# Performance work log

Hardware: AMD Instinct MI355X
Metric: run time of the kernel (lower is better)

The kernel has to match this reference:

```python
import jax, jax.numpy as jnp
import numpy as np

N, E, F_IN, HID, EPS = 50000, 800000, 128, 256, 1e-5

def _glorot(key, shape):
    scale = 1.0 / np.sqrt(shape[0])
    return jax.random.uniform(key, shape, jnp.float32, -scale, scale)

def setup_inputs() -> dict:
    key = jax.random.key(0)
    ks = jax.random.split(key, 20)
    x = jax.random.normal(ks[0], (N, F_IN), jnp.float32)
    edge_index = jax.random.randint(ks[1], (2, E), 0, N, jnp.int64)
    inp = {"x": x, "edge_index": edge_index}
    dims = [F_IN, HID, HID]
    for i in range(3):
        d_in = dims[i]
        inp[f"Wn{i}"] = _glorot(ks[2 + 4 * i], (d_in, HID))      # lin_l weight (neighbors), with bias
        inp[f"bn{i}"] = jnp.zeros((HID,), jnp.float32)
        inp[f"Wr{i}"] = _glorot(ks[3 + 4 * i], (d_in, HID))      # lin_r weight (root), no bias
        inp[f"g{i}"] = jnp.ones((HID,), jnp.float32)              # BN gamma
        inp[f"b{i}"] = jnp.zeros((HID,), jnp.float32)             # BN beta
    return inp

def _sage_bn_elu(x, src, dst, Wn, bn, Wr, g, b):
    # mean aggregation of source features onto destination nodes
    agg = jax.ops.segment_sum(x[src], dst, num_segments=N)                      # [N, d_in]
    deg = jax.ops.segment_sum(jnp.ones((src.shape[0],), x.dtype), dst, num_segments=N)
    agg = agg / jnp.maximum(deg, 1.0)[:, None]
    h = agg @ Wn + bn + x @ Wr                                                  # SAGEConv(root_weight=True)
    mu = jnp.mean(h, axis=0)
    var = jnp.mean((h - mu) ** 2, axis=0)                                       # biased var (BN training)
    h = (h - mu) * jax.lax.rsqrt(var + EPS) * g + b
    return jnp.where(h > 0, h, jnp.expm1(h))                                    # ELU(alpha=1)

def reference(x, edge_index, Wn0, bn0, Wr0, g0, b0, Wn1, bn1, Wr1, g1, b1, Wn2, bn2, Wr2, g2, b2):
    src, dst = edge_index[0], edge_index[1]
    h = _sage_bn_elu(x, src, dst, Wn0, bn0, Wr0, g0, b0)
    h = _sage_bn_elu(h, src, dst, Wn1, bn1, Wr1, g1, b1)
    h = _sage_bn_elu(h, src, dst, Wn2, bn2, Wr2, g2, b2)
    return h
```

## Files before the change

kernel.cpp:

```cpp
#include <hip/hip_runtime.h>
#include <math.h>

#define N_NODES 50000
#define N_EDGES 800000
#define F_IN    128
#define HID     256
#define BN_EPS  1e-5f
#define SCAN_BLOCKS ((N_NODES + 255) / 256)
#define RB256       ((N_NODES + 255) / 256)
#define CAST_BLOCKS (N_NODES * F_IN / 4 / 256)
#define WT_BLOCKS   (16 + 32 + 32)

typedef unsigned int uint;
typedef __attribute__((ext_vector_type(8))) short bf16x8;
typedef __attribute__((ext_vector_type(4))) float f32x4;

__device__ __forceinline__ float bf2f(unsigned short u) {
    return __uint_as_float((uint)u << 16);
}
__device__ __forceinline__ unsigned short f2bf(float f) {
    uint u = __float_as_uint(f);
    return (unsigned short)((u + 0x7FFFu + ((u >> 16) & 1u)) >> 16);
}

__device__ __forceinline__ void gload16(const unsigned short* g, unsigned short* l) {
    __builtin_amdgcn_global_load_lds(
        (const __attribute__((address_space(1))) void*)g,
        (__attribute__((address_space(3))) void*)l, 16, 0, 0);
}

__device__ __forceinline__ void acc_u4(float* a, uint4 v) {
    a[0] += bf2f((unsigned short)(v.x & 0xFFFF)); a[1] += bf2f((unsigned short)(v.x >> 16));
    a[2] += bf2f((unsigned short)(v.y & 0xFFFF)); a[3] += bf2f((unsigned short)(v.y >> 16));
    a[4] += bf2f((unsigned short)(v.z & 0xFFFF)); a[5] += bf2f((unsigned short)(v.z >> 16));
    a[6] += bf2f((unsigned short)(v.w & 0xFFFF)); a[7] += bf2f((unsigned short)(v.w >> 16));
}
__device__ __forceinline__ void acc_u4m(float* a, uint4 v, float m) {
    a[0] += m * bf2f((unsigned short)(v.x & 0xFFFF)); a[1] += m * bf2f((unsigned short)(v.x >> 16));
    a[2] += m * bf2f((unsigned short)(v.y & 0xFFFF)); a[3] += m * bf2f((unsigned short)(v.y >> 16));
    a[4] += m * bf2f((unsigned short)(v.z & 0xFFFF)); a[5] += m * bf2f((unsigned short)(v.z >> 16));
    a[6] += m * bf2f((unsigned short)(v.w & 0xFFFF)); a[7] += m * bf2f((unsigned short)(v.w >> 16));
}

__global__ __launch_bounds__(256) void prep_kernel(
    const float* __restrict__ x, unsigned short* __restrict__ xb,
    const float* __restrict__ Wn0, const float* __restrict__ Wr0, unsigned short* __restrict__ WT0,
    const float* __restrict__ Wn1, const float* __restrict__ Wr1, unsigned short* __restrict__ WT1,
    const float* __restrict__ Wn2, const float* __restrict__ Wr2, unsigned short* __restrict__ WT2,
    int* __restrict__ deg) {
    int bb = blockIdx.x;
    if (bb < CAST_BLOCKS) {
        int i = bb * 256 + threadIdx.x;
        float4 v = *(const float4*)&x[(long)i * 4];
        unsigned short o[4] = {f2bf(v.x), f2bf(v.y), f2bf(v.z), f2bf(v.w)};
        *(uint2*)&xb[(long)i * 4] = *(const uint2*)o;
    } else if (bb < CAST_BLOCKS + SCAN_BLOCKS) {
        int i = (bb - CAST_BLOCKS) * 256 + threadIdx.x;
        if (i < N_NODES) deg[i] = 0;
    } else {
        int wb = bb - (CAST_BLOCKS + SCAN_BLOCKS);
        const float* Wn; const float* Wr; unsigned short* WT; int K1, KT, kb;
        if (wb < 16)      { Wn = Wn0; Wr = Wr0; WT = WT0; K1 = F_IN; KT = 2 * F_IN; kb = wb; }
        else if (wb < 48) { Wn = Wn1; Wr = Wr1; WT = WT1; K1 = HID;  KT = 2 * HID;  kb = wb - 16; }
        else              { Wn = Wn2; Wr = Wr2; WT = WT2; K1 = HID;  KT = 2 * HID;  kb = wb - 48; }
        int n  = threadIdx.x;
        int k0 = kb * 16;
        unsigned short o[16];
#pragma unroll
        for (int j = 0; j < 16; ++j) {
            int k = k0 + j;
            float v = (k < K1) ? Wn[k * HID + n] : Wr[(k - K1) * HID + n];
            o[j] = f2bf(v);
        }
        *(uint4*)&WT[(long)n * KT + k0]     = *(const uint4*)&o[0];
        *(uint4*)&WT[(long)n * KT + k0 + 8] = *(const uint4*)&o[8];
    }
}

__global__ void hist_kernel(const int* __restrict__ dst, int* __restrict__ deg,
                            int* __restrict__ rank) {
    int e = blockIdx.x * blockDim.x + threadIdx.x;
    if (e < N_EDGES) rank[e] = atomicAdd(&deg[dst[e]], 1);
}

__global__ __launch_bounds__(256) void scan1_kernel(const int* __restrict__ deg,
                                                    int* __restrict__ row_ptr,
                                                    int* __restrict__ partials) {
    __shared__ int sm[256];
    int i = blockIdx.x * 256 + threadIdx.x;
    int v = (i < N_NODES) ? deg[i] : 0;
    sm[threadIdx.x] = v;
    __syncthreads();
    for (int off = 1; off < 256; off <<= 1) {
        int t = (threadIdx.x >= off) ? sm[threadIdx.x - off] : 0;
        __syncthreads();
        sm[threadIdx.x] += t;
        __syncthreads();
    }
    if (i < N_NODES) row_ptr[i] = sm[threadIdx.x] - v;
    if (threadIdx.x == 255) partials[blockIdx.x] = sm[255];
}

__global__ __launch_bounds__(256) void scan3_kernel(int* __restrict__ row_ptr,
                                                    const int* __restrict__ partials) {
    __shared__ int red[4];
    int t = threadIdx.x;
    int v = (t < SCAN_BLOCKS && t < (int)blockIdx.x) ? partials[t] : 0;
#pragma unroll
    for (int off = 32; off; off >>= 1) v += __shfl_down(v, off);
    if ((t & 63) == 0) red[t >> 6] = v;
    __syncthreads();
    int base = red[0] + red[1] + red[2] + red[3];
    int i = blockIdx.x * 256 + t;
    if (i < N_NODES) row_ptr[i] += base;
    if (i == 0) row_ptr[N_NODES] = N_EDGES;
}

__global__ void fill_kernel(const int* __restrict__ src, const int* __restrict__ dst,
                            const int* __restrict__ rank, const int* __restrict__ row_ptr,
                            int* __restrict__ csr_src) {
    int e = blockIdx.x * blockDim.x + threadIdx.x;
    if (e >= N_EDGES) return;
    int pos = row_ptr[dst[e]] + rank[e];
    __builtin_nontemporal_store(src[e], &csr_src[pos]);
}

template<int D>
__global__ __launch_bounds__(256) void gather_mean_kernel(
    const unsigned short* __restrict__ x, const int* __restrict__ row_ptr,
    const int* __restrict__ csr_src, unsigned short* __restrict__ agg) {
    int node = blockIdx.x * 4 + (threadIdx.x >> 6);
    int lane = threadIdx.x & 63;
    if (node >= N_NODES) return;
    int beg = row_ptr[node], end = row_ptr[node + 1];
    float acc[8];
#pragma unroll
    for (int j = 0; j < 8; j++) acc[j] = 0.f;
    int e = beg;

    if constexpr (D == 256) {
        const int half = lane >> 5;
        const long lo  = (long)(lane & 31) * 8;
        for (; e + 16 <= end; e += 16) {
            int s0 = csr_src[e + half],      s1 = csr_src[e + 2 + half];
            int s2 = csr_src[e + 4 + half],  s3 = csr_src[e + 6 + half];
            int s4 = csr_src[e + 8 + half],  s5 = csr_src[e + 10 + half];
            int s6 = csr_src[e + 12 + half], s7 = csr_src[e + 14 + half];
            uint4 v0 = *(const uint4*)&x[(long)s0 * 256 + lo];
            uint4 v1 = *(const uint4*)&x[(long)s1 * 256 + lo];
            uint4 v2 = *(const uint4*)&x[(long)s2 * 256 + lo];
            uint4 v3 = *(const uint4*)&x[(long)s3 * 256 + lo];
            uint4 v4 = *(const uint4*)&x[(long)s4 * 256 + lo];
            uint4 v5 = *(const uint4*)&x[(long)s5 * 256 + lo];
            uint4 v6 = *(const uint4*)&x[(long)s6 * 256 + lo];
            uint4 v7 = *(const uint4*)&x[(long)s7 * 256 + lo];
            acc_u4(acc, v0); acc_u4(acc, v1); acc_u4(acc, v2); acc_u4(acc, v3);
            acc_u4(acc, v4); acc_u4(acc, v5); acc_u4(acc, v6); acc_u4(acc, v7);
        }
        for (; e + 8 <= end; e += 8) {
            int s0 = csr_src[e + half],     s1 = csr_src[e + 2 + half];
            int s2 = csr_src[e + 4 + half], s3 = csr_src[e + 6 + half];
            uint4 v0 = *(const uint4*)&x[(long)s0 * 256 + lo];
            uint4 v1 = *(const uint4*)&x[(long)s1 * 256 + lo];
            uint4 v2 = *(const uint4*)&x[(long)s2 * 256 + lo];
            uint4 v3 = *(const uint4*)&x[(long)s3 * 256 + lo];
            acc_u4(acc, v0); acc_u4(acc, v1); acc_u4(acc, v2); acc_u4(acc, v3);
        }
        for (; e + 2 <= end; e += 2) {
            int s0 = csr_src[e + half];
            uint4 v0 = *(const uint4*)&x[(long)s0 * 256 + lo];
            acc_u4(acc, v0);
        }
        if (e < end) {
            int s0 = csr_src[e];
            uint4 v0 = *(const uint4*)&x[(long)s0 * 256 + lo];
            acc_u4m(acc, v0, (half == 0) ? 1.f : 0.f);
        }
#pragma unroll
        for (int j = 0; j < 8; j++) acc[j] += __shfl_xor(acc[j], 32);
        float inv = 1.0f / fmaxf((float)(end - beg), 1.0f);
        if (half == 0) {
            unsigned short ov[8];
#pragma unroll
            for (int j = 0; j < 8; j++) ov[j] = f2bf(acc[j] * inv);
            *(uint4*)&agg[(long)node * 256 + lo] = *(const uint4*)ov;
        }
    } else {
        const int grp = lane >> 4;
        const long lo = (long)(lane & 15) * 8;
        for (; e + 16 <= end; e += 16) {
            int sA = csr_src[e + grp],     sB = csr_src[e + 4 + grp];
            int sC = csr_src[e + 8 + grp], sD = csr_src[e + 12 + grp];
            uint4 vA = *(const uint4*)&x[(long)sA * 128 + lo];
            uint4 vB = *(const uint4*)&x[(long)sB * 128 + lo];
            uint4 vC = *(const uint4*)&x[(long)sC * 128 + lo];
            uint4 vD = *(const uint4*)&x[(long)sD * 128 + lo];
            acc_u4(acc, vA); acc_u4(acc, vB); acc_u4(acc, vC); acc_u4(acc, vD);
        }
        for (; e + 8 <= end; e += 8) {
            int sA = csr_src[e + grp], sB = csr_src[e + 4 + grp];
            uint4 vA = *(const uint4*)&x[(long)sA * 128 + lo];
            uint4 vB = *(const uint4*)&x[(long)sB * 128 + lo];
            acc_u4(acc, vA); acc_u4(acc, vB);
        }
        for (; e + 4 <= end; e += 4) {
            int sA = csr_src[e + grp];
            uint4 vA = *(const uint4*)&x[(long)sA * 128 + lo];
            acc_u4(acc, vA);
        }
        for (; e < end; e++) {
            int s0 = csr_src[e];
            uint4 v0 = *(const uint4*)&x[(long)s0 * 128 + lo];
            acc_u4m(acc, v0, (grp == 0) ? 1.f : 0.f);
        }
#pragma unroll
        for (int j = 0; j < 8; j++) {
            acc[j] += __shfl_xor(acc[j], 32);
            acc[j] += __shfl_xor(acc[j], 16);
        }
        float inv = 1.0f / fmaxf((float)(end - beg), 1.0f);
        if (lane < 16) {
            unsigned short ov[8];
#pragma unroll
            for (int j = 0; j < 8; j++) ov[j] = f2bf(acc[j] * inv);
            *(uint4*)&agg[(long)node * 128 + lo] = *(const uint4*)ov;
        }
    }
}

template<int K1, int K2>
__global__ __launch_bounds__(512) void mfma_gemm_kernel(
    const unsigned short* __restrict__ A1, const unsigned short* __restrict__ A2,
    const unsigned short* __restrict__ WT, const float* __restrict__ bias,
    unsigned short* __restrict__ Hout, float* __restrict__ sred) {
    constexpr int KT = K1 + K2;
    constexpr int NITER = KT / 64;
    __shared__ unsigned short As[2][256 * 64];
    __shared__ unsigned short Bs[2][256 * 64];

    const int tid  = threadIdx.x;
    const int wave = tid >> 6;
    const int lane = tid & 63;
    const int m16  = lane & 15;
    const int quad = lane >> 4;
    const int WR   = wave >> 2;
    const int WC   = wave & 3;
    const int r0   = blockIdx.x * 256;
    const int rl = lane >> 3;
    const int cl = lane & 7;
    const int csw = cl ^ rl;

    f32x4 acc[8][4];
#pragma unroll
    for (int mt = 0; mt < 8; mt++)
#pragma unroll
        for (int nt = 0; nt < 4; nt++) acc[mt][nt] = (f32x4){0.f, 0.f, 0.f, 0.f};

    auto issue = [&](int t) {
        const int buf = t & 1;
        const int k0  = t * 64;
        const unsigned short* Ab;
        int pitch, kk;
        if (k0 < K1) { Ab = A1; pitch = K1; kk = k0; }
        else         { Ab = A2; pitch = K2; kk = k0 - K1; }
#pragma unroll
        for (int j = 0; j < 4; ++j) {
            int lr = wave * 32 + j * 8 + rl;
            long gr = min(r0 + lr, N_NODES - 1);
            gload16(&Ab[gr * pitch + kk + csw * 8], &As[buf][(wave * 32 + j * 8) * 64]);
        }
#pragma unroll
        for (int j = 0; j < 4; ++j) {
            long gn = wave * 32 + j * 8 + rl;
            gload16(&WT[gn * KT + k0 + csw * 8], &Bs[buf][(wave * 32 + j * 8) * 64]);
        }
    };

    issue(0);

#pragma unroll
    for (int it = 0; it < NITER; ++it) {
        const int cur = it & 1;
        if (it + 1 < NITER) {
            issue(it + 1);
            asm volatile("s_waitcnt vmcnt(8)" ::: "memory");
        } else {
            asm volatile("s_waitcnt vmcnt(0)" ::: "memory");
        }
        __builtin_amdgcn_s_barrier();
#pragma unroll
        for (int ks = 0; ks < 2; ++ks) {
            bf16x8 afrag[8], bfrag[4];
#pragma unroll
            for (int mt = 0; mt < 8; mt++) {
                int ar = WR * 128 + mt * 16 + m16;
                afrag[mt] = *(const bf16x8*)&As[cur][ar * 64 + (((ks * 4 + quad) ^ (m16 & 7)) * 8)];
            }
#pragma unroll
            for (int nt = 0; nt < 4; nt++) {
                int br = WC * 64 + nt * 16 + m16;
                bfrag[nt] = *(const bf16x8*)&Bs[cur][br * 64 + (((ks * 4 + quad) ^ (m16 & 7)) * 8)];
            }
#pragma unroll
            for (int mt = 0; mt < 8; mt++)
#pragma unroll
                for (int nt = 0; nt < 4; nt++)
                    acc[mt][nt] = __builtin_amdgcn_mfma_f32_16x16x32_bf16(
                        afrag[mt], bfrag[nt], acc[mt][nt], 0, 0, 0);
        }
        __builtin_amdgcn_s_barrier();
    }

#pragma unroll
    for (int nt = 0; nt < 4; nt++) {
        int lcol = WC * 64 + nt * 16 + m16;
        float bv = bias[lcol];
        float s = 0.f, q = 0.f;
#pragma unroll
        for (int mt = 0; mt < 8; mt++) {
#pragma unroll
            for (int reg = 0; reg < 4; reg++) {
                int row = r0 + WR * 128 + mt * 16 + quad * 4 + reg;
                float v = acc[mt][nt][reg] + bv;
                if (row < N_NODES) {
                    Hout[(long)row * HID + lcol] = f2bf(v);
                    s += v;
                    q += v * v;
                }
            }
        }
        s += __shfl_xor(s, 16); s += __shfl_xor(s, 32);
        q += __shfl_xor(q, 16); q += __shfl_xor(q, 32);
        if (quad == 0) {
            float* base = &sred[(long)(blockIdx.x * 2 + WR) * 512];
            base[lcol]       = s;
            base[256 + lcol] = q;
        }
    }
}

__global__ __launch_bounds__(512) void bn_reduce_kernel(const float* __restrict__ sred,
                                                        const float* __restrict__ g,
                                                        const float* __restrict__ b,
                                                        float* __restrict__ ss, int nrows) {
    __shared__ float qsm[256];
    int t  = threadIdx.x;
    int ch = t & 255;
    int off = (t < 256) ? 0 : 256;
    float S0 = 0.f, S1 = 0.f, S2 = 0.f, S3 = 0.f;
    int rb = 0;
    for (; rb + 4 <= nrows; rb += 4) {
        S0 += sred[(long)(rb + 0) * 512 + off + ch];
        S1 += sred[(long)(rb + 1) * 512 + off + ch];
        S2 += sred[(long)(rb + 2) * 512 + off + ch];
        S3 += sred[(long)(rb + 3) * 512 + off + ch];
    }
    for (; rb < nrows; rb++) S0 += sred[(long)rb * 512 + off + ch];
    float Sv = (S0 + S1) + (S2 + S3);
    if (t >= 256) qsm[ch] = Sv;
    __syncthreads();
    if (t < 256) {
        float mu  = Sv * (1.0f / N_NODES);
        float var = qsm[ch] * (1.0f / N_NODES) - mu * mu;
        var = fmaxf(var, 0.f);
        float sc = rsqrtf(var + BN_EPS) * g[ch];
        ss[ch]       = sc;
        ss[HID + ch] = b[ch] - mu * sc;
    }
}

template<bool OUT32>
__global__ void bn_elu_kernel(const unsigned short* __restrict__ h, const float* __restrict__ ss,
                              void* __restrict__ out) {
    const int total4 = N_NODES * HID / 4;
    int i = blockIdx.x * blockDim.x + threadIdx.x;
    if (i >= total4) return;
    int c4 = (i % (HID / 4)) * 4;
    uint2 v = *(const uint2*)&h[(long)i * 4];
    float4 sc = *(const float4*)&ss[c4];
    float4 sh = *(const float4*)&ss[HID + c4];
    float in[4] = {bf2f((unsigned short)(v.x & 0xFFFF)), bf2f((unsigned short)(v.x >> 16)),
                   bf2f((unsigned short)(v.y & 0xFFFF)), bf2f((unsigned short)(v.y >> 16))};
    float scv[4] = {sc.x, sc.y, sc.z, sc.w};
    float shv[4] = {sh.x, sh.y, sh.z, sh.w};
    float o[4];
#pragma unroll
    for (int j = 0; j < 4; j++) {
        float t = fmaf(in[j], scv[j], shv[j]);
        o[j] = t > 0.f ? t : expm1f(t);
    }
    if (OUT32) {
        float4 ov = {o[0], o[1], o[2], o[3]};
        *(float4*)&((float*)out)[(long)i * 4] = ov;
    } else {
        unsigned short ov[4] = {f2bf(o[0]), f2bf(o[1]), f2bf(o[2]), f2bf(o[3])};
        *(uint2*)&((unsigned short*)out)[(long)i * 4] = *(const uint2*)ov;
    }
}

extern "C" void kernel_launch(void* const* d_in, const int* in_sizes, int n_in,
                              void* d_out, int out_size, void* d_ws, size_t ws_size,
                              hipStream_t stream) {
    const float* x   = (const float*)d_in[0];
    const int*   ei  = (const int*)d_in[1];
    const int*   src = ei;
    const int*   dst = ei + N_EDGES;
    const float* Wn[3] = {(const float*)d_in[2],  (const float*)d_in[7],  (const float*)d_in[12]};
    const float* bn[3] = {(const float*)d_in[3],  (const float*)d_in[8],  (const float*)d_in[13]};
    const float* Wr[3] = {(const float*)d_in[4],  (const float*)d_in[9],  (const float*)d_in[14]};
    const float* g [3] = {(const float*)d_in[5],  (const float*)d_in[10], (const float*)d_in[15]};
    const float* b [3] = {(const float*)d_in[6],  (const float*)d_in[11], (const float*)d_in[16]};
    float* out = (float*)d_out;

    const size_t BF = (size_t)N_NODES * HID * 2;
    char* ws = (char*)d_ws;
    unsigned short* B0  = (unsigned short*)(ws);
    unsigned short* B1  = (unsigned short*)(ws + BF);
    unsigned short* B2  = (unsigned short*)(ws + 2 * BF);
    unsigned short* XB  = (unsigned short*)(ws + 3 * BF);
    char* ws2 = ws + 3 * BF + (size_t)N_NODES * F_IN * 2;
    unsigned short* WT0 = (unsigned short*)(ws2);
    unsigned short* WT1 = (unsigned short*)(ws2 + 256 * 256 * 2);
    unsigned short* WT2 = (unsigned short*)(ws2 + 256 * 256 * 2 + 256 * 512 * 2);
    char* ws3 = ws2 + 256 * 256 * 2 + 2 * (256 * 512 * 2);
    int*   row_ptr = (int*)ws3;
    int*   deg_i   = row_ptr + (N_NODES + 1);
    int*   partial = deg_i + N_NODES;
    int*   rank    = partial + SCAN_BLOCKS;
    int*   csr_src = rank + N_EDGES;
    float* sred    = (float*)(csr_src + N_EDGES);
    float* ss      = sred + (size_t)2 * RB256 * 512;

    const int eb = (N_EDGES + 255) / 256;
    const int gather_blocks = (N_NODES + 3) / 4;
    const int elu_blocks = (N_NODES * HID / 4 + 255) / 256;
    const int prep_blocks = CAST_BLOCKS + SCAN_BLOCKS + WT_BLOCKS;

    prep_kernel<<<prep_blocks, 256, 0, stream>>>(x, XB,
        Wn[0], Wr[0], WT0, Wn[1], Wr[1], WT1, Wn[2], Wr[2], WT2, deg_i);
    hist_kernel<<<eb, 256, 0, stream>>>(dst, deg_i, rank);
    scan1_kernel<<<SCAN_BLOCKS, 256, 0, stream>>>(deg_i, row_ptr, partial);
    scan3_kernel<<<SCAN_BLOCKS, 256, 0, stream>>>(row_ptr, partial);
    fill_kernel<<<eb, 256, 0, stream>>>(src, dst, rank, row_ptr, csr_src);

    gather_mean_kernel<F_IN><<<gather_blocks, 256, 0, stream>>>(XB, row_ptr, csr_src, B0);
    mfma_gemm_kernel<F_IN, F_IN><<<RB256, 512, 0, stream>>>(B0, XB, WT0, bn[0], B1, sred);
    bn_reduce_kernel<<<1, 512, 0, stream>>>(sred, g[0], b[0], ss, 2 * RB256);
    bn_elu_kernel<false><<<elu_blocks, 256, 0, stream>>>(B1, ss, B2);

    gather_mean_kernel<HID><<<gather_blocks, 256, 0, stream>>>(B2, row_ptr, csr_src, B0);
    mfma_gemm_kernel<HID, HID><<<RB256, 512, 0, stream>>>(B0, B2, WT1, bn[1], B1, sred);
    bn_reduce_kernel<<<1, 512, 0, stream>>>(sred, g[1], b[1], ss, 2 * RB256);
    bn_elu_kernel<false><<<elu_blocks, 256, 0, stream>>>(B1, ss, B2);

    gather_mean_kernel<HID><<<gather_blocks, 256, 0, stream>>>(B2, row_ptr, csr_src, B0);
    mfma_gemm_kernel<HID, HID><<<RB256, 512, 0, stream>>>(B0, B2, WT2, bn[2], B1, sred);
    bn_reduce_kernel<<<1, 512, 0, stream>>>(sred, g[2], b[2], ss, 2 * RB256);
    bn_elu_kernel<true><<<elu_blocks, 256, 0, stream>>>(B1, ss, out);
}
```

Before: 545.6 us.

## Split GEMM into 128x128 tiles with column halves for more blocks

Shrinks each GEMM block from a 256x256 output tile with 8 waves to a 128x128 tile with 4 waves. The grid becomes row blocks times two column halves. This raises the block count well above the CU count, aiming to fill the GPU better where it was previously underfilled. The BN partial-sum layout and the reduce kernel are reworked to match. In exchange, activation and weight tiles are reloaded more often and per-wave register reuse is smaller.

```diff
diff --git a/kernel.cpp b/kernel.cpp
--- a/kernel.cpp
+++ b/kernel.cpp
@@ -7,7 +7,7 @@
 #define HID     256
 #define BN_EPS  1e-5f
 #define SCAN_BLOCKS ((N_NODES + 255) / 256)
-#define RB256       ((N_NODES + 255) / 256)
+#define RB128       ((N_NODES + 127) / 128)
 #define CAST_BLOCKS (N_NODES * F_IN / 4 / 256)
 #define WT_BLOCKS   (16 + 32 + 32)
 
@@ -229,30 +229,32 @@
 }
 
 template<int K1, int K2>
-__global__ __launch_bounds__(512) void mfma_gemm_kernel(
+__global__ __launch_bounds__(256) void mfma_gemm_kernel(
     const unsigned short* __restrict__ A1, const unsigned short* __restrict__ A2,
     const unsigned short* __restrict__ WT, const float* __restrict__ bias,
     unsigned short* __restrict__ Hout, float* __restrict__ sred) {
     constexpr int KT = K1 + K2;
     constexpr int NITER = KT / 64;
-    __shared__ unsigned short As[2][256 * 64];
-    __shared__ unsigned short Bs[2][256 * 64];
+    __shared__ unsigned short As[2][128 * 64];
+    __shared__ unsigned short Bs[2][128 * 64];
 
     const int tid  = threadIdx.x;
     const int wave = tid >> 6;
     const int lane = tid & 63;
     const int m16  = lane & 15;
     const int quad = lane >> 4;
-    const int WR   = wave >> 2;
-    const int WC   = wave & 3;
-    const int r0   = blockIdx.x * 256;
+    const int WR   = wave >> 1;
+    const int WC   = wave & 1;
+    const int row_block = blockIdx.x >> 1;
+    const int col_half  = blockIdx.x & 1;
+    const int r0   = row_block * 128;
     const int rl = lane >> 3;
     const int cl = lane & 7;
     const int csw = cl ^ rl;
 
-    f32x4 acc[8][4];
-#pragma unroll
-    for (int mt = 0; mt < 8; mt++)
+    f32x4 acc[4][4];
+#pragma unroll
+    for (int mt = 0; mt < 4; mt++)
 #pragma unroll
         for (int nt = 0; nt < 4; nt++) acc[mt][nt] = (f32x4){0.f, 0.f, 0.f, 0.f};
 
@@ -271,7 +273,7 @@
         }
 #pragma unroll
         for (int j = 0; j < 4; ++j) {
-            long gn = wave * 32 + j * 8 + rl;
+            long gn = col_half * 128 + wave * 32 + j * 8 + rl;
             gload16(&WT[gn * KT + k0 + csw * 8], &Bs[buf][(wave * 32 + j * 8) * 64]);
         }
     };
@@ -290,10 +292,10 @@
         __builtin_amdgcn_s_barrier();
 #pragma unroll
         for (int ks = 0; ks < 2; ++ks) {
-            bf16x8 afrag[8], bfrag[4];
-#pragma unroll
-            for (int mt = 0; mt < 8; mt++) {
-                int ar = WR * 128 + mt * 16 + m16;
+            bf16x8 afrag[4], bfrag[4];
+#pragma unroll
+            for (int mt = 0; mt < 4; mt++) {
+                int ar = WR * 64 + mt * 16 + m16;
                 afrag[mt] = *(const bf16x8*)&As[cur][ar * 64 + (((ks * 4 + quad) ^ (m16 & 7)) * 8)];
             }
 #pragma unroll
@@ -302,7 +304,7 @@
                 bfrag[nt] = *(const bf16x8*)&Bs[cur][br * 64 + (((ks * 4 + quad) ^ (m16 & 7)) * 8)];
             }
 #pragma unroll
-            for (int mt = 0; mt < 8; mt++)
+            for (int mt = 0; mt < 4; mt++)
 #pragma unroll
                 for (int nt = 0; nt < 4; nt++)
                     acc[mt][nt] = __builtin_amdgcn_mfma_f32_16x16x32_bf16(
@@ -314,16 +316,17 @@
 #pragma unroll
     for (int nt = 0; nt < 4; nt++) {
         int lcol = WC * 64 + nt * 16 + m16;
-        float bv = bias[lcol];
+        int col  = col_half * 128 + lcol;
+        float bv = bias[col];
         float s = 0.f, q = 0.f;
 #pragma unroll
-        for (int mt = 0; mt < 8; mt++) {
+        for (int mt = 0; mt < 4; mt++) {
 #pragma unroll
             for (int reg = 0; reg < 4; reg++) {
-                int row = r0 + WR * 128 + mt * 16 + quad * 4 + reg;
+                int row = r0 + WR * 64 + mt * 16 + quad * 4 + reg;
                 float v = acc[mt][nt][reg] + bv;
                 if (row < N_NODES) {
-                    Hout[(long)row * HID + lcol] = f2bf(v);
+                    Hout[(long)row * HID + col] = f2bf(v);
                     s += v;
                     q += v * v;
                 }
@@ -332,9 +335,9 @@
         s += __shfl_xor(s, 16); s += __shfl_xor(s, 32);
         q += __shfl_xor(q, 16); q += __shfl_xor(q, 32);
         if (quad == 0) {
-            float* base = &sred[(long)(blockIdx.x * 2 + WR) * 512];
+            float* base = &sred[(long)(blockIdx.x * 2 + WR) * 256];
             base[lcol]       = s;
-            base[256 + lcol] = q;
+            base[128 + lcol] = q;
         }
     }
 }
@@ -342,20 +345,28 @@
 __global__ __launch_bounds__(512) void bn_reduce_kernel(const float* __restrict__ sred,
                                                         const float* __restrict__ g,
                                                         const float* __restrict__ b,
-                                                        float* __restrict__ ss, int nrows) {
+                                                        float* __restrict__ ss) {
     __shared__ float qsm[256];
-    int t  = threadIdx.x;
-    int ch = t & 255;
-    int off = (t < 256) ? 0 : 256;
+    int t   = threadIdx.x;
+    int ch  = t & 255;
+    int off = (t < 256) ? 0 : 128;
+    int chh = ch >> 7;
+    int lc  = ch & 127;
     float S0 = 0.f, S1 = 0.f, S2 = 0.f, S3 = 0.f;
     int rb = 0;
-    for (; rb + 4 <= nrows; rb += 4) {
-        S0 += sred[(long)(rb + 0) * 512 + off + ch];
-        S1 += sred[(long)(rb + 1) * 512 + off + ch];
-        S2 += sred[(long)(rb + 2) * 512 + off + ch];
-        S3 += sred[(long)(rb + 3) * 512 + off + ch];
-    }
-    for (; rb < nrows; rb++) S0 += sred[(long)rb * 512 + off + ch];
+    for (; rb + 2 <= RB128; rb += 2) {
+        long base0 = (long)(((rb + 0) * 2 + chh) * 2) * 256 + off + lc;
+        long base1 = (long)(((rb + 1) * 2 + chh) * 2) * 256 + off + lc;
+        S0 += sred[base0];
+        S1 += sred[base0 + 256];
+        S2 += sred[base1];
+        S3 += sred[base1 + 256];
+    }
+    for (; rb < RB128; rb++) {
+        long base0 = (long)((rb * 2 + chh) * 2) * 256 + off + lc;
+        S0 += sred[base0];
+        S1 += sred[base0 + 256];
+    }
     float Sv = (S0 + S1) + (S2 + S3);
     if (t >= 256) qsm[ch] = Sv;
     __syncthreads();
@@ -429,12 +440,13 @@
     int*   rank    = partial + SCAN_BLOCKS;
     int*   csr_src = rank + N_EDGES;
     float* sred    = (float*)(csr_src + N_EDGES);
-    float* ss      = sred + (size_t)2 * RB256 * 512;
+    float* ss      = sred + (size_t)RB128 * 2 * 2 * 256;
 
     const int eb = (N_EDGES + 255) / 256;
     const int gather_blocks = (N_NODES + 3) / 4;
     const int elu_blocks = (N_NODES * HID / 4 + 255) / 256;
     const int prep_blocks = CAST_BLOCKS + SCAN_BLOCKS + WT_BLOCKS;
+    const int gemm_blocks = RB128 * 2;
 
     prep_kernel<<<prep_blocks, 256, 0, stream>>>(x, XB,
         Wn[0], Wr[0], WT0, Wn[1], Wr[1], WT1, Wn[2], Wr[2], WT2, deg_i);
@@ -444,17 +456,17 @@
     fill_kernel<<<eb, 256, 0, stream>>>(src, dst, rank, row_ptr, csr_src);
 
     gather_mean_kernel<F_IN><<<gather_blocks, 256, 0, stream>>>(XB, row_ptr, csr_src, B0);
-    mfma_gemm_kernel<F_IN, F_IN><<<RB256, 512, 0, stream>>>(B0, XB, WT0, bn[0], B1, sred);
-    bn_reduce_kernel<<<1, 512, 0, stream>>>(sred, g[0], b[0], ss, 2 * RB256);
+    mfma_gemm_kernel<F_IN, F_IN><<<gemm_blocks, 256, 0, stream>>>(B0, XB, WT0, bn[0], B1, sred);
+    bn_reduce_kernel<<<1, 512, 0, stream>>>(sred, g[0], b[0], ss);
     bn_elu_kernel<false><<<elu_blocks, 256, 0, stream>>>(B1, ss, B2);
 
     gather_mean_kernel<HID><<<gather_blocks, 256, 0, stream>>>(B2, row_ptr, csr_src, B0);
-    mfma_gemm_kernel<HID, HID><<<RB256, 512, 0, stream>>>(B0, B2, WT1, bn[1], B1, sred);
-    bn_reduce_kernel<<<1, 512, 0, stream>>>(sred, g[1], b[1], ss, 2 * RB256);
+    mfma_gemm_kernel<HID, HID><<<gemm_blocks, 256, 0, stream>>>(B0, B2, WT1, bn[1], B1, sred);
+    bn_reduce_kernel<<<1, 512, 0, stream>>>(sred, g[1], b[1], ss);
     bn_elu_kernel<false><<<elu_blocks, 256, 0, stream>>>(B1, ss, B2);
 
     gather_mean_kernel<HID><<<gather_blocks, 256, 0, stream>>>(B2, row_ptr, csr_src, B0);
-    mfma_gemm_kernel<HID, HID><<<RB256, 512, 0, stream>>>(B0, B2, WT2, bn[2], B1, sred);
-    bn_reduce_kernel<<<1, 512, 0, stream>>>(sred, g[2], b[2], ss, 2 * RB256);
+    mfma_gemm_kernel<HID, HID><<<gemm_blocks, 256, 0, stream>>>(B0, B2, WT2, bn[2], B1, sred);
+    bn_reduce_kernel<<<1, 512, 0, stream>>>(sred, g[2], b[2], ss);
     bn_elu_kernel<true><<<elu_blocks, 256, 0, stream>>>(B1, ss, out);
 }
```

Measured after the change: 531.5 us. 1.03x faster.
